# Performance work log

Measured on AMD Instinct MI355X. Metric: run time of the kernel, lower is better.

The kernel has to match this reference:

```python
import jax, jax.numpy as jnp
import numpy as np

B, L, D, H, R = 4, 4096, 1024, 16, 30
DK = D // H  # 64
EPS = 1e-12  # torch F.normalize eps


def setup_inputs() -> dict:
    key = jax.random.key(0)
    ks = jax.random.split(key, 16)
    n = lambda k, shp, s=0.02: jax.random.normal(k, shp, jnp.float32) * s
    return {
        "queries": jax.random.normal(ks[0], (B, L, D), jnp.float32),
        "keys": jax.random.normal(ks[1], (B, L, D), jnp.float32),
        "values": jax.random.normal(ks[2], (B, L, D), jnp.float32),
        # linear weights stored as (in, out); equivalent to torch y = x @ W.T + b
        "Wq": n(ks[3], (D, D)), "bq": jnp.zeros((D,), jnp.float32),
        "Wk": n(ks[4], (D, D)), "bk": jnp.zeros((D,), jnp.float32),
        "We": n(ks[5], (H, DK, R), 0.1),
        "Wr": n(ks[6], (H, DK, R), 0.1),
        "Lam": jax.random.uniform(ks[7], (H, R), jnp.float32),
        "Wc": n(ks[8], (2 * R, DK)), "bc": jnp.zeros((DK,), jnp.float32),
        "Wo": n(ks[9], (D, D)), "bo": jnp.zeros((D,), jnp.float32),
    }


def _l2norm(x):
    nrm = jnp.sqrt(jnp.sum(x * x, axis=-1, keepdims=True))
    return x / jnp.maximum(nrm, EPS)


def reference(queries, keys, values, Wq, bq, Wk, bk, We, Wr, Lam, Wc, bc, Wo, bo):
    b, l, _ = queries.shape
    # projections -> [B, H, L, DK]
    q = (queries @ Wq + bq).reshape(b, l, H, DK).transpose(0, 2, 1, 3)
    k = (keys @ Wk + bk).reshape(b, l, H, DK).transpose(0, 2, 1, 3)
    # causal cumulative mean over sequence
    normal = (jnp.arange(l, dtype=jnp.float32) + 1.0)[None, None, :, None]
    q = jnp.cumsum(q, axis=2) / normal
    k = jnp.cumsum(k, axis=2) / normal
    # L2-normalized feature map
    q = _l2norm(q)
    k = _l2norm(k)
    # per-head low-rank projections -> [B, H, L, R]
    escore = jnp.einsum('bhld,hdr->bhlr', q, We)
    rscore = jnp.einsum('bhld,hdr->bhlr', k, Wr)
    score = jnp.concatenate([escore, rscore], axis=-1)  # [B, H, L, 2R]
    out = score @ Wc + bc                                # [B, H, L, DK]
    out = out.transpose(0, 2, 1, 3).reshape(b, l, H * DK)
    out = out @ Wo + bo                                  # [B, L, D]
    # dropout is identity in eval mode
    return (out, escore, rscore, Lam)
```

## Files before the change

kernel.cpp:

```cpp
#include <hip/hip_runtime.h>
#include <hip/hip_bf16.h>

#define BATCH 4
#define LSEQ 4096
#define DMODEL 1024
#define NHEAD 16
#define RDIM 30
#define DKH 64
#define NCHUNK 32
#define CHUNK 128

typedef __attribute__((ext_vector_type(8))) short bf16x8_t;
typedef __attribute__((ext_vector_type(4))) float f32x4_t;

static __device__ __forceinline__ unsigned short f2bf(float f) {
    __hip_bfloat16 h = __float2bfloat16(f);
    unsigned short u;
    __builtin_memcpy(&u, &h, 2);
    return u;
}
static __device__ __forceinline__ float b2f(unsigned short u) {
    unsigned v = ((unsigned)u) << 16;
    float f;
    __builtin_memcpy(&f, &v, 4);
    return f;
}

#define SWAIT_VM8()   { asm volatile("s_waitcnt vmcnt(8)" ::: "memory"); __builtin_amdgcn_sched_barrier(0); }
#define SWAIT_VM4()   { asm volatile("s_waitcnt vmcnt(4)" ::: "memory"); __builtin_amdgcn_sched_barrier(0); }
#define SWAIT_VM0()   { asm volatile("s_waitcnt vmcnt(0)" ::: "memory"); __builtin_amdgcn_sched_barrier(0); }
#define SWAIT_LGKM0() { asm volatile("s_waitcnt lgkmcnt(0)" ::: "memory"); __builtin_amdgcn_sched_barrier(0); }
#define SBARRIER()    { __builtin_amdgcn_s_barrier(); __builtin_amdgcn_sched_barrier(0); }

__global__ void transpose_cvt_kernel(const float* __restrict__ W, unsigned short* __restrict__ outT,
                                     int Kd, int Nd) {
    __shared__ float tile[32][33];
    int n0 = blockIdx.x * 32, k0 = blockIdx.y * 32;
    int tx = threadIdx.x, ty = threadIdx.y;
    #pragma unroll
    for (int r = ty; r < 32; r += 8)
        tile[r][tx] = W[(size_t)(k0 + r) * Nd + n0 + tx];
    __syncthreads();
    #pragma unroll
    for (int r = ty; r < 32; r += 8)
        outT[(size_t)(n0 + r) * Kd + k0 + tx] = f2bf(tile[tx][r]);
}

__global__ void wpack_kernel(const float* __restrict__ We, const float* __restrict__ Wr,
                             unsigned short* __restrict__ WeP, unsigned short* __restrict__ WrP) {
    int h = blockIdx.x;
    const float* W = blockIdx.y ? Wr : We;
    unsigned short* O = blockIdx.y ? WrP : WeP;
    for (int idx = threadIdx.x; idx < 2048; idx += 256) {
        int col = idx >> 6, k = idx & 63;
        float v = (col < RDIM) ? W[((size_t)h * 64 + k) * RDIM + col] : 0.f;
        O[((size_t)h << 11) + idx] = f2bf(v);
    }
}

__global__ __launch_bounds__(256) void wfold_kernel(
    const float* __restrict__ Wc, const float* __restrict__ Wo,
    unsigned short* __restrict__ WfoldT)
{
    __shared__ float WoT[64][65];
    __shared__ float WcT[64][61];
    const int tid = threadIdx.x;
    const int n0 = blockIdx.x * 64, h = blockIdx.y;
    for (int i = tid; i < 4096; i += 256) {
        int dk = i >> 6, n = i & 63;
        WoT[dk][n] = Wo[(size_t)(h * 64 + dk) * DMODEL + n0 + n];
    }
    for (int i = tid; i < 3840; i += 256) {
        int j = i >> 6, dk = i & 63;
        WcT[dk][j] = Wc[j * 64 + dk];
    }
    __syncthreads();
    #pragma unroll 1
    for (int oo = 0; oo < 16; ++oo) {
        int n = (tid >> 6) + oo * 4;
        int j = tid & 63;
        int jr = (j < 30) ? j : (j >= 32 && j < 62) ? (j - 2) : -1;
        float acc = 0.f;
        if (jr >= 0) {
            #pragma unroll
            for (int dk = 0; dk < 64; ++dk)
                acc = fmaf(WcT[dk][jr], WoT[dk][n], acc);
        }
        WfoldT[(size_t)(n0 + n) * 1024 + h * 64 + j] = f2bf(acc);
    }
}

__global__ void bias2_kernel(const float* __restrict__ Wo, const float* __restrict__ bc,
                             const float* __restrict__ bo, float* __restrict__ bias2) {
    int n = blockIdx.x * 256 + threadIdx.x;
    float a = bo[n];
    for (int d = 0; d < DMODEL; ++d)
        a = fmaf(bc[d & 63], Wo[(size_t)d * DMODEL + n], a);
    bias2[n] = a;
}

#define GBM 256
#define GBN 256
#define GBK 64
#define NTILES 16

template <bool AF32, bool BF16_OUT>
__global__ __launch_bounds__(512, 2) void gemm8_kernel(
    const void* __restrict__ Av0, const void* __restrict__ Av1,
    const unsigned short* __restrict__ Bt0, const unsigned short* __restrict__ Bt1,
    const float* __restrict__ bias0, const float* __restrict__ bias1,
    void* __restrict__ Cv0, void* __restrict__ Cv1,
    int N)
{
    __shared__ __align__(16) unsigned short As[2][GBM * GBK];
    __shared__ __align__(16) unsigned short Bs[2][GBM * GBK];
    const int tid = threadIdx.x;
    const int lane = tid & 63;
    const int wid = tid >> 6;
    const int wm = wid >> 2;
    const int wn = wid & 3;
    const int lm = lane & 15;
    const int kb = lane >> 4;
    const int z = blockIdx.z;

    const void* Av = z ? Av1 : Av0;
    const unsigned short* Bt = z ? Bt1 : Bt0;
    const float* bias = z ? bias1 : bias0;
    void* Cv = z ? Cv1 : Cv0;

    const int nwg = gridDim.x * gridDim.y;
    const int wg = blockIdx.y * gridDim.x + blockIdx.x;
    const int cpx = nwg >> 3;
    const int swz = (wg & 7) * cpx + (wg >> 3);
    const int bn = swz % gridDim.x;
    const int bm = swz / gridDim.x;

    const unsigned short* Btile = Bt + (size_t)(bn * GBN) * 1024;
    const float* A32_tile = nullptr;
    const unsigned short* A16_tile = nullptr;
    if constexpr (AF32) A32_tile = (const float*)Av + (size_t)(bm * GBM) * 1024;
    else                A16_tile = (const unsigned short*)Av + (size_t)(bm * GBM) * 1024;

    f32x4_t acc[8][4];
    #pragma unroll
    for (int i = 0; i < 8; ++i)
        #pragma unroll
        for (int j = 0; j < 4; ++j)
            acc[i][j] = f32x4_t{0.f, 0.f, 0.f, 0.f};

    auto B_STAGE = [&](int buf, int kt) {
        #pragma unroll
        for (int seg = 0; seg < 4; ++seg) {
            const int s = (seg << 13) + (tid << 4);
            const int row = s >> 7;
            const int cc = ((s >> 4) & 7) ^ (row & 7);
            const unsigned short* gb = Btile + (size_t)row * 1024 + kt * GBK + cc * 8;
            __builtin_amdgcn_global_load_lds(
                (const __attribute__((address_space(1))) void*)gb,
                (__attribute__((address_space(3))) void*)((char*)&Bs[buf][0] + (seg << 13) + (wid << 10)),
                16, 0, 0);
        }
    };
    auto A_STAGE16 = [&](int buf, int kt) {
        #pragma unroll
        for (int seg = 0; seg < 4; ++seg) {
            const int s = (seg << 13) + (tid << 4);
            const int row = s >> 7;
            const int cc = ((s >> 4) & 7) ^ (row & 7);
            const unsigned short* ga = A16_tile + (size_t)row * 1024 + kt * GBK + cc * 8;
            __builtin_amdgcn_global_load_lds(
                (const __attribute__((address_space(1))) void*)ga,
                (__attribute__((address_space(3))) void*)((char*)&As[buf][0] + (seg << 13) + (wid << 10)),
                16, 0, 0);
        }
    };
    float4 areg[8];
    auto A_ISSUE = [&](int kt) {
        #pragma unroll
        for (int p = 0; p < 8; ++p) {
            int q = p * 512 + tid;
            int row = q >> 4, kq = q & 15;
            areg[p] = *(const float4*)(A32_tile + (size_t)row * 1024 + kt * GBK + kq * 4);
        }
    };
    auto A_WRITE = [&](int buf) {
        #pragma unroll
        for (int p = 0; p < 8; ++p) {
            int q = p * 512 + tid;
            int row = q >> 4, kq = q & 15;
            ushort4 pk;
            pk.x = f2bf(areg[p].x); pk.y = f2bf(areg[p].y);
            pk.z = f2bf(areg[p].z); pk.w = f2bf(areg[p].w);
            int cc = (kq >> 1) ^ (row & 7);
            *(ushort4*)((char*)&As[buf][0] + row * 128 + (cc << 4) + (kq & 1) * 8) = pk;
        }
    };

    bf16x8_t af[8], bfr[4];
    auto LOADFRAGS = [&](int buf, int ks) {
        #pragma unroll
        for (int i = 0; i < 8; ++i) {
            int row = wm * 128 + i * 16 + lm;
            int cc = (ks * 4 + kb) ^ (row & 7);
            af[i] = *(const bf16x8_t*)((const char*)&As[buf][0] + row * 128 + cc * 16);
        }
        #pragma unroll
        for (int j = 0; j < 4; ++j) {
            int row = wn * 64 + j * 16 + lm;
            int cc = (ks * 4 + kb) ^ (row & 7);
            bfr[j] = *(const bf16x8_t*)((const char*)&Bs[buf][0] + row * 128 + cc * 16);
        }
    };
    auto MFMAC = [&]() {
        __builtin_amdgcn_s_setprio(1);
        #pragma unroll
        for (int i = 0; i < 8; ++i)
            #pragma unroll
            for (int j = 0; j < 4; ++j)
                acc[i][j] = __builtin_amdgcn_mfma_f32_16x16x32_bf16(af[i], bfr[j], acc[i][j], 0, 0, 0);
        __builtin_amdgcn_s_setprio(0);
    };

    if constexpr (AF32) {
        B_STAGE(0, 0);
        A_ISSUE(0);
        SWAIT_VM0();
        A_WRITE(0);
        B_STAGE(1, 1);
        A_ISSUE(1);
        SWAIT_LGKM0();
        SBARRIER();
    } else {
        A_STAGE16(0, 0);
        B_STAGE(0, 0);
        __builtin_amdgcn_sched_barrier(0);
        A_STAGE16(1, 1);
        B_STAGE(1, 1);
        SWAIT_VM8();
        SBARRIER();
    }

    int cur = 0;
    for (int t = 0; t < NTILES; ++t) {
        LOADFRAGS(cur, 0);
        MFMAC();
        LOADFRAGS(cur, 1);
        SWAIT_LGKM0();
        SBARRIER();
        if constexpr (AF32) {
            if (t + 2 < NTILES) B_STAGE(cur, t + 2);
            if (t + 1 < NTILES) {
                if (t + 2 < NTILES) { SWAIT_VM4(); }
                else                { SWAIT_VM0(); }
                A_WRITE(cur ^ 1);
                if (t + 2 < NTILES) A_ISSUE(t + 2);
            }
            MFMAC();
            if (t + 1 < NTILES) { SWAIT_LGKM0(); SBARRIER(); }
        } else {
            if (t + 2 < NTILES) { A_STAGE16(cur, t + 2); B_STAGE(cur, t + 2); }
            MFMAC();
            if (t + 1 < NTILES) {
                if (t + 2 < NTILES) { SWAIT_VM8(); }
                else                { SWAIT_VM0(); }
                SBARRIER();
            }
        }
        cur ^= 1;
    }

    #pragma unroll
    for (int i = 0; i < 8; ++i) {
        int row = bm * GBM + wm * 128 + i * 16 + (lane >> 4) * 4;
        #pragma unroll
        for (int j = 0; j < 4; ++j) {
            int col = bn * GBN + wn * 64 + j * 16 + lm;
            float bv = bias[col];
            #pragma unroll
            for (int r = 0; r < 4; ++r) {
                float v = acc[i][j][r] + bv;
                if constexpr (BF16_OUT)
                    ((unsigned short*)Cv)[(size_t)(row + r) * N + col] = f2bf(v);
                else
                    ((float*)Cv)[(size_t)(row + r) * N + col] = v;
            }
        }
    }
}

__global__ __launch_bounds__(256) void cumsum_local_kernel(
    unsigned short* __restrict__ Qb, unsigned short* __restrict__ Kb,
    float* __restrict__ partQ, float* __restrict__ partK)
{
    const int tid = threadIdx.x;
    const int c = blockIdx.x;
    const int bz = blockIdx.y;
    const int b = bz >> 1;
    unsigned short* buf = (bz & 1) ? Kb : Qb;
    float* part = (bz & 1) ? partK : partQ;
    size_t base = ((size_t)(b * LSEQ + c * CHUNK)) * DMODEL + tid * 4;
    float rx = 0.f, ry = 0.f, rz = 0.f, rw = 0.f;
    #pragma unroll 4
    for (int i = 0; i < CHUNK; ++i) {
        ushort4 v = *(ushort4*)(buf + base + (size_t)i * DMODEL);
        rx += b2f(v.x); ry += b2f(v.y); rz += b2f(v.z); rw += b2f(v.w);
        ushort4 o;
        o.x = f2bf(rx); o.y = f2bf(ry); o.z = f2bf(rz); o.w = f2bf(rw);
        *(ushort4*)(buf + base + (size_t)i * DMODEL) = o;
    }
    float4 p = make_float4(rx, ry, rz, rw);
    *(float4*)(part + ((size_t)(b * NCHUNK + c)) * DMODEL + tid * 4) = p;
}

__global__ void chunk_offsets_kernel(float* __restrict__ partQ, float* __restrict__ partK)
{
    int t = blockIdx.x * 256 + threadIdx.x;
    float* part = blockIdx.y ? partK : partQ;
    int b = t >> 10, d = t & 1023;
    float run = 0.f;
    #pragma unroll
    for (int c = 0; c < NCHUNK; ++c) {
        size_t idx = ((size_t)(b * NCHUNK + c)) * DMODEL + d;
        float v = part[idx];
        part[idx] = run;
        run += v;
    }
}

__global__ __launch_bounds__(256) void score_kernel(
    const unsigned short* __restrict__ Qc, const unsigned short* __restrict__ Kc,
    const float* __restrict__ partQ, const float* __restrict__ partK,
    const unsigned short* __restrict__ WeP, const unsigned short* __restrict__ WrP,
    float* __restrict__ escore, float* __restrict__ rscore,
    unsigned short* __restrict__ sbf)
{
    __shared__ float n2buf[4][64];
    const int tid = threadIdx.x;
    const int lane = tid & 63;
    const int w = tid >> 6;
    const int lm = lane & 15;
    const int lk = lane >> 4;
    const int c = blockIdx.x;
    const int bh = blockIdx.y;
    const int z = blockIdx.z;
    const int b = bh >> 4, h = bh & 15;
    const unsigned short* X = z ? Kc : Qc;
    const float* part = z ? partK : partQ;
    const unsigned short* WP = z ? WrP : WeP;
    float* eout = z ? rscore : escore;
    const int row0 = c * 256 + w * 64;
    const int co = c * 2 + (w >> 1);

    const float* offp = part + ((size_t)(b * NCHUNK + co)) * DMODEL + h * 64 + lk * 8;
    float o0[8], o1[8];
    {
        float4 a = *(const float4*)(offp);
        float4 bb = *(const float4*)(offp + 4);
        float4 cc = *(const float4*)(offp + 32);
        float4 dd = *(const float4*)(offp + 36);
        o0[0] = a.x; o0[1] = a.y; o0[2] = a.z; o0[3] = a.w;
        o0[4] = bb.x; o0[5] = bb.y; o0[6] = bb.z; o0[7] = bb.w;
        o1[0] = cc.x; o1[1] = cc.y; o1[2] = cc.z; o1[3] = cc.w;
        o1[4] = dd.x; o1[5] = dd.y; o1[6] = dd.z; o1[7] = dd.w;
    }

    const unsigned short* wpb = WP + ((size_t)h << 11) + lm * 64 + lk * 8;
    bf16x8_t b00 = *(const bf16x8_t*)(wpb);
    bf16x8_t b01 = *(const bf16x8_t*)(wpb + 32);
    bf16x8_t b10 = *(const bf16x8_t*)(wpb + 16 * 64);
    bf16x8_t b11 = *(const bf16x8_t*)(wpb + 16 * 64 + 32);

    f32x4_t acc[4][2];
    float n2p[4];
    #pragma unroll
    for (int i = 0; i < 4; ++i) {
        n2p[i] = 0.f;
        acc[i][0] = f32x4_t{0.f, 0.f, 0.f, 0.f};
        acc[i][1] = f32x4_t{0.f, 0.f, 0.f, 0.f};
    }

    const unsigned short* xbase = X + ((size_t)(b * LSEQ + row0 + lm)) * DMODEL + h * 64 + lk * 8;
    #pragma unroll
    for (int i = 0; i < 4; ++i) {
        const unsigned short* xp = xbase + (size_t)(16 * i) * DMODEL;
        bf16x8_t x0 = *(const bf16x8_t*)(xp);
        bf16x8_t x1 = *(const bf16x8_t*)(xp + 32);
        bf16x8_t xa0, xa1;
        #pragma unroll
        for (int j = 0; j < 8; ++j) {
            float xf = b2f((unsigned short)x0[j]) + o0[j];
            n2p[i] = fmaf(xf, xf, n2p[i]);
            xa0[j] = (short)f2bf(xf);
        }
        #pragma unroll
        for (int j = 0; j < 8; ++j) {
            float xf = b2f((unsigned short)x1[j]) + o1[j];
            n2p[i] = fmaf(xf, xf, n2p[i]);
            xa1[j] = (short)f2bf(xf);
        }
        acc[i][0] = __builtin_amdgcn_mfma_f32_16x16x32_bf16(xa0, b00, acc[i][0], 0, 0, 0);
        acc[i][1] = __builtin_amdgcn_mfma_f32_16x16x32_bf16(xa0, b10, acc[i][1], 0, 0, 0);
        acc[i][0] = __builtin_amdgcn_mfma_f32_16x16x32_bf16(xa1, b01, acc[i][0], 0, 0, 0);
        acc[i][1] = __builtin_amdgcn_mfma_f32_16x16x32_bf16(xa1, b11, acc[i][1], 0, 0, 0);
    }

    #pragma unroll
    for (int i = 0; i < 4; ++i) {
        n2p[i] += __shfl_xor(n2p[i], 16);
        n2p[i] += __shfl_xor(n2p[i], 32);
    }
    if (lane < 16) {
        #pragma unroll
        for (int i = 0; i < 4; ++i) n2buf[w][16 * i + lane] = n2p[i];
    }
    __syncthreads();

    #pragma unroll
    for (int i = 0; i < 4; ++i) {
        f32x4_t n2v = *(const f32x4_t*)&n2buf[w][16 * i + lk * 4];
        float inv[4];
        #pragma unroll
        for (int r = 0; r < 4; ++r) {
            int lr = row0 + 16 * i + lk * 4 + r;
            inv[r] = 1.f / fmaxf(sqrtf(n2v[r]), 1e-12f * (float)(lr + 1));
        }
        #pragma unroll
        for (int j = 0; j < 2; ++j) {
            int col = 16 * j + lm;
            #pragma unroll
            for (int r = 0; r < 4; ++r) {
                int lr = row0 + 16 * i + lk * 4 + r;
                float v = acc[i][j][r] * inv[r];
                if (col < RDIM)
                    eout[(((size_t)(b * NHEAD + h)) * LSEQ + lr) * RDIM + col] = v;
                sbf[((size_t)(b * LSEQ + lr)) * 1024 + h * 64 + z * 32 + col] =
                    (col < RDIM) ? f2bf(v) : (unsigned short)0;
            }
        }
    }
}

extern "C" void kernel_launch(void* const* d_in, const int* in_sizes, int n_in,
                              void* d_out, int out_size, void* d_ws, size_t ws_size,
                              hipStream_t stream)
{
    const float* queries = (const float*)d_in[0];
    const float* keys    = (const float*)d_in[1];
    const float* Wq = (const float*)d_in[3];
    const float* bq = (const float*)d_in[4];
    const float* Wk = (const float*)d_in[5];
    const float* bk = (const float*)d_in[6];
    const float* We = (const float*)d_in[7];
    const float* Wr = (const float*)d_in[8];
    const float* Lam = (const float*)d_in[9];
    const float* Wc = (const float*)d_in[10];
    const float* bc = (const float*)d_in[11];
    const float* Wo = (const float*)d_in[12];
    const float* bo = (const float*)d_in[13];

    float* out = (float*)d_out;
    float* escore = out + (size_t)16777216;
    float* rscore = out + (size_t)24641536;
    float* lam_out = out + (size_t)32505856;

    char* ws = (char*)d_ws;
    unsigned short* sbf = (unsigned short*)ws;
    unsigned short* Qb  = (unsigned short*)(ws + 33554432);
    unsigned short* Kb  = (unsigned short*)(ws + 67108864);
    unsigned short* WqT = (unsigned short*)(ws + 100663296);
    unsigned short* WkT = (unsigned short*)(ws + 102760448);
    unsigned short* WfT = (unsigned short*)(ws + 104857600);
    float* bias2 = (float*)(ws + 106954752);
    float* partQ = (float*)(ws + 106958848);
    float* partK = (float*)(ws + 107483136);
    unsigned short* WeP = (unsigned short*)(ws + 108007424);
    unsigned short* WrP = (unsigned short*)(ws + 108072960);

    dim3 tb(32, 8);
    transpose_cvt_kernel<<<dim3(32, 32), tb, 0, stream>>>(Wq, WqT, DMODEL, DMODEL);
    transpose_cvt_kernel<<<dim3(32, 32), tb, 0, stream>>>(Wk, WkT, DMODEL, DMODEL);
    wpack_kernel<<<dim3(16, 2), 256, 0, stream>>>(We, Wr, WeP, WrP);
    wfold_kernel<<<dim3(16, 16), 256, 0, stream>>>(Wc, Wo, WfT);
    bias2_kernel<<<4, 256, 0, stream>>>(Wo, bc, bo, bias2);

    gemm8_kernel<true, true><<<dim3(4, 64, 2), 512, 0, stream>>>(
        queries, keys, WqT, WkT, bq, bk, Qb, Kb, 1024);

    cumsum_local_kernel<<<dim3(NCHUNK, 8), 256, 0, stream>>>(Qb, Kb, partQ, partK);
    chunk_offsets_kernel<<<dim3(16, 2), 256, 0, stream>>>(partQ, partK);

    score_kernel<<<dim3(16, 64, 2), 256, 0, stream>>>(Qb, Kb, partQ, partK, WeP, WrP,
                                                      escore, rscore, sbf);

    gemm8_kernel<false, false><<<dim3(4, 64, 1), 512, 0, stream>>>(
        sbf, sbf, WfT, WfT, bias2, bias2, out, out, 1024);

    hipMemcpyAsync(lam_out, Lam, 480 * sizeof(float), hipMemcpyDeviceToDevice, stream);
}
```

Measured before the change: 277.1 us.

## Fuse chunk-local cumsum into QK projection GEMM epilogue

Moves the within-chunk prefix sum of Q and K projections into the GEMM epilogue. Each wave scans its 128-row slab in registers using cross-lane shuffles and writes the chunk totals for the offset pass. This removes the separate cumsum kernel, which re-read and rewrote the full bf16 Q/K buffers. It also merges the two weight transpose launches into one. The scan now sums fp32 values before rounding to bf16, which slightly changes numerics, and it relies on each wave covering exactly one 128-row chunk.

```diff
diff --git a/kernel.cpp b/kernel.cpp
--- a/kernel.cpp
+++ b/kernel.cpp
@@ -32,18 +32,20 @@
 #define SWAIT_LGKM0() { asm volatile("s_waitcnt lgkmcnt(0)" ::: "memory"); __builtin_amdgcn_sched_barrier(0); }
 #define SBARRIER()    { __builtin_amdgcn_s_barrier(); __builtin_amdgcn_sched_barrier(0); }
 
-__global__ void transpose_cvt_kernel(const float* __restrict__ W, unsigned short* __restrict__ outT,
-                                     int Kd, int Nd) {
+__global__ void transpose_cvt_kernel(const float* __restrict__ W0, const float* __restrict__ W1,
+                                     unsigned short* __restrict__ O0, unsigned short* __restrict__ O1) {
     __shared__ float tile[32][33];
+    const float* W = blockIdx.z ? W1 : W0;
+    unsigned short* outT = blockIdx.z ? O1 : O0;
     int n0 = blockIdx.x * 32, k0 = blockIdx.y * 32;
     int tx = threadIdx.x, ty = threadIdx.y;
     #pragma unroll
     for (int r = ty; r < 32; r += 8)
-        tile[r][tx] = W[(size_t)(k0 + r) * Nd + n0 + tx];
+        tile[r][tx] = W[(size_t)(k0 + r) * DMODEL + n0 + tx];
     __syncthreads();
     #pragma unroll
     for (int r = ty; r < 32; r += 8)
-        outT[(size_t)(n0 + r) * Kd + k0 + tx] = f2bf(tile[tx][r]);
+        outT[(size_t)(n0 + r) * DMODEL + k0 + tx] = f2bf(tile[tx][r]);
 }
 
 __global__ void wpack_kernel(const float* __restrict__ We, const float* __restrict__ Wr,
@@ -101,19 +103,19 @@
 
 #define GBM 256
 #define GBN 256
-#define GBK 64
 #define NTILES 16
 
-template <bool AF32, bool BF16_OUT>
+template <bool AF32, bool BF16_OUT, bool DOCUM>
 __global__ __launch_bounds__(512, 2) void gemm8_kernel(
     const void* __restrict__ Av0, const void* __restrict__ Av1,
     const unsigned short* __restrict__ Bt0, const unsigned short* __restrict__ Bt1,
     const float* __restrict__ bias0, const float* __restrict__ bias1,
     void* __restrict__ Cv0, void* __restrict__ Cv1,
+    float* __restrict__ part0, float* __restrict__ part1,
     int N)
 {
-    __shared__ __align__(16) unsigned short As[2][GBM * GBK];
-    __shared__ __align__(16) unsigned short Bs[2][GBM * GBK];
+    __shared__ __align__(16) unsigned short As[2][GBM * 64];
+    __shared__ __align__(16) unsigned short Bs[2][GBM * 64];
     const int tid = threadIdx.x;
     const int lane = tid & 63;
     const int wid = tid >> 6;
@@ -127,6 +129,7 @@
     const unsigned short* Bt = z ? Bt1 : Bt0;
     const float* bias = z ? bias1 : bias0;
     void* Cv = z ? Cv1 : Cv0;
+    float* part = z ? part1 : part0;
 
     const int nwg = gridDim.x * gridDim.y;
     const int wg = blockIdx.y * gridDim.x + blockIdx.x;
@@ -154,7 +157,7 @@
             const int s = (seg << 13) + (tid << 4);
             const int row = s >> 7;
             const int cc = ((s >> 4) & 7) ^ (row & 7);
-            const unsigned short* gb = Btile + (size_t)row * 1024 + kt * GBK + cc * 8;
+            const unsigned short* gb = Btile + (size_t)row * 1024 + kt * 64 + cc * 8;
             __builtin_amdgcn_global_load_lds(
                 (const __attribute__((address_space(1))) void*)gb,
                 (__attribute__((address_space(3))) void*)((char*)&Bs[buf][0] + (seg << 13) + (wid << 10)),
@@ -167,7 +170,7 @@
             const int s = (seg << 13) + (tid << 4);
             const int row = s >> 7;
             const int cc = ((s >> 4) & 7) ^ (row & 7);
-            const unsigned short* ga = A16_tile + (size_t)row * 1024 + kt * GBK + cc * 8;
+            const unsigned short* ga = A16_tile + (size_t)row * 1024 + kt * 64 + cc * 8;
             __builtin_amdgcn_global_load_lds(
                 (const __attribute__((address_space(1))) void*)ga,
                 (__attribute__((address_space(3))) void*)((char*)&As[buf][0] + (seg << 13) + (wid << 10)),
@@ -180,7 +183,7 @@
         for (int p = 0; p < 8; ++p) {
             int q = p * 512 + tid;
             int row = q >> 4, kq = q & 15;
-            areg[p] = *(const float4*)(A32_tile + (size_t)row * 1024 + kt * GBK + kq * 4);
+            areg[p] = *(const float4*)(A32_tile + (size_t)row * 1024 + kt * 64 + kq * 4);
         }
     };
     auto A_WRITE = [&](int buf) {
@@ -269,47 +272,58 @@
         cur ^= 1;
     }
 
-    #pragma unroll
-    for (int i = 0; i < 8; ++i) {
-        int row = bm * GBM + wm * 128 + i * 16 + (lane >> 4) * 4;
+    if constexpr (DOCUM) {
+        const int g = lane >> 4;
+        const int row0 = bm * GBM + wm * 128;
         #pragma unroll
         for (int j = 0; j < 4; ++j) {
-            int col = bn * GBN + wn * 64 + j * 16 + lm;
-            float bv = bias[col];
+            const int col = bn * GBN + wn * 64 + j * 16 + lm;
+            const float bv = bias[col];
+            float runbase = 0.f;
             #pragma unroll
-            for (int r = 0; r < 4; ++r) {
-                float v = acc[i][j][r] + bv;
-                if constexpr (BF16_OUT)
-                    ((unsigned short*)Cv)[(size_t)(row + r) * N + col] = f2bf(v);
-                else
-                    ((float*)Cv)[(size_t)(row + r) * N + col] = v;
+            for (int i = 0; i < 8; ++i) {
+                float c0 = acc[i][j][0] + bv;
+                float c1 = c0 + acc[i][j][1] + bv;
+                float c2 = c1 + acc[i][j][2] + bv;
+                float c3 = c2 + acc[i][j][3] + bv;
+                float tot = c3;
+                float x16 = __shfl_xor(tot, 16);
+                float x32 = __shfl_xor(tot, 32);
+                float x48 = __shfl_xor(x16, 32);
+                float pre = (g == 1) ? x16
+                          : (g == 2) ? (x32 + x48)
+                          : (g == 3) ? (x16 + x32 + x48) : 0.f;
+                float base2 = runbase + pre;
+                runbase += tot + x16 + x32 + x48;
+                int row = row0 + i * 16 + g * 4;
+                unsigned short* cp = (unsigned short*)Cv + (size_t)row * N + col;
+                cp[0]         = f2bf(base2 + c0);
+                cp[(size_t)N] = f2bf(base2 + c1);
+                cp[(size_t)2 * N] = f2bf(base2 + c2);
+                cp[(size_t)3 * N] = f2bf(base2 + c3);
             }
-        }
-    }
-}
-
-__global__ __launch_bounds__(256) void cumsum_local_kernel(
-    unsigned short* __restrict__ Qb, unsigned short* __restrict__ Kb,
-    float* __restrict__ partQ, float* __restrict__ partK)
-{
-    const int tid = threadIdx.x;
-    const int c = blockIdx.x;
-    const int bz = blockIdx.y;
-    const int b = bz >> 1;
-    unsigned short* buf = (bz & 1) ? Kb : Qb;
-    float* part = (bz & 1) ? partK : partQ;
-    size_t base = ((size_t)(b * LSEQ + c * CHUNK)) * DMODEL + tid * 4;
-    float rx = 0.f, ry = 0.f, rz = 0.f, rw = 0.f;
-    #pragma unroll 4
-    for (int i = 0; i < CHUNK; ++i) {
-        ushort4 v = *(ushort4*)(buf + base + (size_t)i * DMODEL);
-        rx += b2f(v.x); ry += b2f(v.y); rz += b2f(v.z); rw += b2f(v.w);
-        ushort4 o;
-        o.x = f2bf(rx); o.y = f2bf(ry); o.z = f2bf(rz); o.w = f2bf(rw);
-        *(ushort4*)(buf + base + (size_t)i * DMODEL) = o;
-    }
-    float4 p = make_float4(rx, ry, rz, rw);
-    *(float4*)(part + ((size_t)(b * NCHUNK + c)) * DMODEL + tid * 4) = p;
+            if (g == 0)
+                part[((size_t)(row0 >> 7) << 10) + col] = runbase;
+        }
+    } else {
+        #pragma unroll
+        for (int i = 0; i < 8; ++i) {
+            int row = bm * GBM + wm * 128 + i * 16 + (lane >> 4) * 4;
+            #pragma unroll
+            for (int j = 0; j < 4; ++j) {
+                int col = bn * GBN + wn * 64 + j * 16 + lm;
+                float bv = bias[col];
+                #pragma unroll
+                for (int r = 0; r < 4; ++r) {
+                    float v = acc[i][j][r] + bv;
+                    if constexpr (BF16_OUT)
+                        ((unsigned short*)Cv)[(size_t)(row + r) * N + col] = f2bf(v);
+                    else
+                        ((float*)Cv)[(size_t)(row + r) * N + col] = v;
+                }
+            }
+        }
+    }
 }
 
 __global__ void chunk_offsets_kernel(float* __restrict__ partQ, float* __restrict__ partK)
@@ -477,23 +491,21 @@
     unsigned short* WrP = (unsigned short*)(ws + 108072960);
 
     dim3 tb(32, 8);
-    transpose_cvt_kernel<<<dim3(32, 32), tb, 0, stream>>>(Wq, WqT, DMODEL, DMODEL);
-    transpose_cvt_kernel<<<dim3(32, 32), tb, 0, stream>>>(Wk, WkT, DMODEL, DMODEL);
+    transpose_cvt_kernel<<<dim3(32, 32, 2), tb, 0, stream>>>(Wq, Wk, WqT, WkT);
     wpack_kernel<<<dim3(16, 2), 256, 0, stream>>>(We, Wr, WeP, WrP);
     wfold_kernel<<<dim3(16, 16), 256, 0, stream>>>(Wc, Wo, WfT);
     bias2_kernel<<<4, 256, 0, stream>>>(Wo, bc, bo, bias2);
 
-    gemm8_kernel<true, true><<<dim3(4, 64, 2), 512, 0, stream>>>(
-        queries, keys, WqT, WkT, bq, bk, Qb, Kb, 1024);
-
-    cumsum_local_kernel<<<dim3(NCHUNK, 8), 256, 0, stream>>>(Qb, Kb, partQ, partK);
+    gemm8_kernel<true, true, true><<<dim3(4, 64, 2), 512, 0, stream>>>(
+        queries, keys, WqT, WkT, bq, bk, Qb, Kb, partQ, partK, 1024);
+
     chunk_offsets_kernel<<<dim3(16, 2), 256, 0, stream>>>(partQ, partK);
 
     score_kernel<<<dim3(16, 64, 2), 256, 0, stream>>>(Qb, Kb, partQ, partK, WeP, WrP,
                                                       escore, rscore, sbf);
 
-    gemm8_kernel<false, false><<<dim3(4, 64, 1), 512, 0, stream>>>(
-        sbf, sbf, WfT, WfT, bias2, bias2, out, out, 1024);
+    gemm8_kernel<false, false, false><<<dim3(4, 64, 1), 512, 0, stream>>>(
+        sbf, sbf, WfT, WfT, bias2, bias2, out, out, nullptr, nullptr, 1024);
 
     hipMemcpyAsync(lam_out, Lam, 480 * sizeof(float), hipMemcpyDeviceToDevice, stream);
 }
```

Measured after the change: 270.0 us. 2.6% less time.
